# Kernel optimization log

Measured on AMD Instinct MI355X. Metric: run time of the kernel, lower is better.

## Reference

```python
import jax, jax.numpy as jnp
import numpy as np

N0, N1, N2 = 320000, 80000, 16000
E1, E2 = 800000, 160000
IN_C, HID, OUT_C = 128, 64, 48
H1, H2 = 4, 1
NEG_SLOPE = 0.2  # PyG GATv2Conv default leaky_relu slope


def _glorot(key, shape):
    fan_in = shape[0]
    return jax.random.normal(key, shape, jnp.float32) / jnp.sqrt(jnp.asarray(fan_in, jnp.float32))


def setup_inputs() -> dict:
    key = jax.random.key(0)
    ks = jax.random.split(key, 12)
    inp = {
        "x": jax.random.normal(ks[0], (N0, IN_C), jnp.float32),
        # layer 1: GATv2Conv(IN_C -> HID, heads=H1, concat=True)
        "Wl1": _glorot(ks[1], (IN_C, H1 * HID)),
        "bl1": jnp.zeros((H1 * HID,), jnp.float32),
        "Wr1": _glorot(ks[2], (IN_C, H1 * HID)),
        "br1": jnp.zeros((H1 * HID,), jnp.float32),
        "att1": jax.random.normal(ks[3], (H1, HID), jnp.float32) * 0.1,
        "bias1": jnp.zeros((H1 * HID,), jnp.float32),
        # layer 2: GATv2Conv(H1*HID -> OUT_C, heads=H2, concat=False)
        "Wl2": _glorot(ks[4], (H1 * HID, H2 * OUT_C)),
        "bl2": jnp.zeros((H2 * OUT_C,), jnp.float32),
        "Wr2": _glorot(ks[5], (H1 * HID, H2 * OUT_C)),
        "br2": jnp.zeros((H2 * OUT_C,), jnp.float32),
        "att2": jax.random.normal(ks[6], (H2, OUT_C), jnp.float32) * 0.1,
        "bias2": jnp.zeros((OUT_C,), jnp.float32),
        # sampled bipartite edge lists (edge j->i: src index into x_src, dst into x_dst)
        "src1": jax.random.randint(ks[7], (E1,), 0, N0, jnp.int32),
        "dst1": jax.random.randint(ks[8], (E1,), 0, N1, jnp.int32),
        "src2": jax.random.randint(ks[9], (E2,), 0, N1, jnp.int32),
        "dst2": jax.random.randint(ks[10], (E2,), 0, N2, jnp.int32),
        "n1": N1,
        "n2": N2,
    }
    return inp


def gatv2_conv(x_src, x_dst, src, dst, Wl, bl, Wr, br, att, bias, n_dst, concat):
    H, C = att.shape
    xl = (x_src @ Wl + bl).reshape(-1, H, C)   # [N_src, H, C] (source transform)
    xr = (x_dst @ Wr + br).reshape(-1, H, C)   # [N_dst, H, C] (target transform)
    e = xl[src] + xr[dst]                      # [E, H, C]
    e = jnp.where(e > 0, e, NEG_SLOPE * e)     # leaky_relu (GATv2: nonlinearity before att)
    alpha = jnp.einsum('ehc,hc->eh', e, att)   # [E, H] attention logits
    # softmax over edges sharing the same target node
    amax = jax.ops.segment_max(alpha, dst, num_segments=n_dst)
    ex = jnp.exp(alpha - amax[dst])
    denom = jax.ops.segment_sum(ex, dst, num_segments=n_dst)
    w = ex / (denom[dst] + 1e-16)              # [E, H]
    out = jax.ops.segment_sum(xl[src] * w[:, :, None], dst, num_segments=n_dst)  # [N_dst, H, C]
    out = out.reshape(n_dst, H * C) if concat else out.mean(axis=1)
    return out + bias


def reference(x, Wl1, bl1, Wr1, br1, att1, bias1, Wl2, bl2, Wr2, br2, att2, bias2,
              src1, dst1, src2, dst2, n1, n2):
    h = gatv2_conv(x, x[:n1], src1, dst1, Wl1, bl1, Wr1, br1, att1, bias1, n1, True)
    h = jax.nn.relu(h)
    # dropout is identity in eval mode
    h = gatv2_conv(h, h[:n2], src2, dst2, Wl2, bl2, Wr2, br2, att2, bias2, n2, False)
    return jax.nn.log_softmax(h, axis=-1)
```

## Files before the change

kernel.cpp:

```cpp
#include <hip/hip_runtime.h>
#include <hip/hip_bf16.h>

#define N0_  320000
#define N1_  80000
#define N2_  16000
#define INC_ 128
#define HID_ 64
#define H1_  4
#define C1_  256
#define OUT_ 48
#define OUTP_ 64
#define NEG_ 0.2f

typedef __attribute__((ext_vector_type(8))) short bfrag8;
typedef __attribute__((ext_vector_type(4))) float ffrag4;

__device__ __forceinline__ float bf2f(unsigned short u){
  unsigned int v = ((unsigned int)u) << 16;
  return __uint_as_float(v);
}
__device__ __forceinline__ unsigned short f2bf(float f){
  unsigned int u = __float_as_uint(f);
  u += 0x7FFFu + ((u >> 16) & 1u);
  return (unsigned short)(u >> 16);
}
__device__ __forceinline__ void unpack2(unsigned int u, float& lo, float& hi){
  lo = __uint_as_float(u << 16);
  hi = __uint_as_float(u & 0xffff0000u);
}

__global__ void transpose_all(const float* __restrict__ Wl1, const float* __restrict__ Wr1,
                              const float* __restrict__ Wl2, const float* __restrict__ Wr2,
                              unsigned short* __restrict__ Wt1l, unsigned short* __restrict__ Wt1r,
                              unsigned short* __restrict__ Wt2l, unsigned short* __restrict__ Wt2r){
  int idx = blockIdx.x*256 + threadIdx.x;
  if (idx < 32768){ int n = idx >> 7, k = idx & 127; Wt1l[idx] = f2bf(Wl1[k*C1_ + n]); }
  else if (idx < 65536){ int j = idx - 32768; int n = j >> 7, k = j & 127; Wt1r[j] = f2bf(Wr1[k*C1_ + n]); }
  else if (idx < 77824){ int j = idx - 65536; int n = j >> 8, k = j & 255; Wt2l[j] = f2bf(Wl2[k*OUT_ + n]); }
  else if (idx < 90112){ int j = idx - 77824; int n = j >> 8, k = j & 255; Wt2r[j] = f2bf(Wr2[k*OUT_ + n]); }
}

__global__ __launch_bounds__(256, 4) void gemm1_split(
    const float* __restrict__ X,
    const unsigned short* __restrict__ Wtl, const unsigned short* __restrict__ Wtr,
    const float* __restrict__ bl, const float* __restrict__ br,
    unsigned short* __restrict__ outl, unsigned short* __restrict__ outr, int nblk_l)
{
  __shared__ unsigned short Buf[8704];
  const int t = threadIdx.x;
  const int lane = t & 63, wave = t >> 6;
  const bool isR = (int)blockIdx.x >= nblk_l;
  const int row0 = (isR ? (int)blockIdx.x - nblk_l : (int)blockIdx.x) << 6;
  const unsigned short* Wt = isR ? Wtr : Wtl;
  const float* bias = isR ? br : bl;
  unsigned short* out = isR ? outr : outl;
  const int l15 = lane & 15, q = lane >> 4;
  const int wcol = wave << 6;
  const int c4 = t & 31;

  #pragma unroll
  for (int i = 0; i < 8; ++i){
    int r = (i<<3) + (t>>5);
    float4 xv = *(const float4*)(X + ((size_t)(row0 + r) << 7) + (c4<<2));
    ushort4 s; s.x=f2bf(xv.x); s.y=f2bf(xv.y); s.z=f2bf(xv.z); s.w=f2bf(xv.w);
    *(ushort4*)(&Buf[r*136 + (c4<<2)]) = s;
  }
  __syncthreads();

  ffrag4 z = {0.f, 0.f, 0.f, 0.f};
  ffrag4 acc[4][4];
  #pragma unroll
  for (int mt = 0; mt < 4; ++mt)
    #pragma unroll
    for (int nt = 0; nt < 4; ++nt) acc[mt][nt] = z;

  #pragma unroll
  for (int ks = 0; ks < 4; ++ks){
    bfrag8 bfr[4];
    #pragma unroll
    for (int nt = 0; nt < 4; ++nt)
      bfr[nt] = *(const bfrag8*)(Wt + (size_t)(wcol + (nt<<4) + l15)*128 + (ks<<5) + (q<<3));
    #pragma unroll
    for (int mt = 0; mt < 4; ++mt){
      bfrag8 af = *(const bfrag8*)(&Buf[((mt<<4) + l15)*136 + (ks<<5) + (q<<3)]);
      #pragma unroll
      for (int nt = 0; nt < 4; ++nt)
        acc[mt][nt] = __builtin_amdgcn_mfma_f32_16x16x32_bf16(af, bfr[nt], acc[mt][nt], 0, 0, 0);
    }
  }

  float bb[4];
  #pragma unroll
  for (int nt = 0; nt < 4; ++nt) bb[nt] = bias[wcol + (nt<<4) + l15];

  #pragma unroll
  for (int h = 0; h < 2; ++h){
    __syncthreads();
    #pragma unroll
    for (int mh = 0; mh < 2; ++mh){
      int mt = (h<<1) + mh;
      #pragma unroll
      for (int nt = 0; nt < 4; ++nt)
        #pragma unroll
        for (int rg = 0; rg < 4; ++rg)
          Buf[((mh<<4) + (q<<2) + rg)*264 + wcol + (nt<<4) + l15] = f2bf(acc[mt][nt][rg] + bb[nt]);
    }
    __syncthreads();
    #pragma unroll
    for (int i = 0; i < 4; ++i){
      int idx = (i<<8) + t;
      int r = idx >> 5, c = (idx & 31) << 3;
      *(bfrag8*)(out + ((size_t)(row0 + (h<<5) + r) << 8) + c) = *(const bfrag8*)(&Buf[r*264 + c]);
    }
  }
}

__global__ __launch_bounds__(256, 4) void gemm2_split(
    const unsigned short* __restrict__ Hin,
    const unsigned short* __restrict__ Wtl, const unsigned short* __restrict__ Wtr,
    const float* __restrict__ bl, const float* __restrict__ br,
    float* __restrict__ outl, float* __restrict__ outr, int nblk_l)
{
  __shared__ unsigned short As2[64*264];
  const int t = threadIdx.x;
  const int lane = t & 63, wave = t >> 6;
  const bool isR = (int)blockIdx.x >= nblk_l;
  const int row0 = (isR ? (int)blockIdx.x - nblk_l : (int)blockIdx.x) << 6;
  const unsigned short* Wt = isR ? Wtr : Wtl;
  const float* bias = isR ? br : bl;
  float* out = isR ? outr : outl;
  const int l15 = lane & 15, q = lane >> 4;

  #pragma unroll
  for (int i = 0; i < 8; ++i){
    int idx = (i<<8) + t;
    int r = idx >> 5, c = (idx & 31) << 3;
    *(bfrag8*)(&As2[r*264 + c]) = *(const bfrag8*)(Hin + ((size_t)(row0 + r) << 8) + c);
  }
  __syncthreads();

  if (wave < 3){
    bfrag8 bfr[8];
    #pragma unroll
    for (int ks = 0; ks < 8; ++ks)
      bfr[ks] = *(const bfrag8*)(Wt + (size_t)((wave<<4) + l15)*256 + (ks<<5) + (q<<3));
    ffrag4 z = {0.f, 0.f, 0.f, 0.f};
    ffrag4 acc[4] = {z, z, z, z};
    #pragma unroll
    for (int ks = 0; ks < 8; ++ks){
      #pragma unroll
      for (int mt = 0; mt < 4; ++mt){
        bfrag8 af = *(const bfrag8*)(&As2[((mt<<4) + l15)*264 + (ks<<5) + (q<<3)]);
        acc[mt] = __builtin_amdgcn_mfma_f32_16x16x32_bf16(af, bfr[ks], acc[mt], 0, 0, 0);
      }
    }
    int col = (wave<<4) + l15;
    float bb = bias[col];
    #pragma unroll
    for (int mt = 0; mt < 4; ++mt)
      #pragma unroll
      for (int rg = 0; rg < 4; ++rg){
        int row = row0 + (mt<<4) + (q<<2) + rg;
        out[(size_t)row*OUTP_ + col] = acc[mt][rg] + bb;
      }
  } else {
    #pragma unroll
    for (int i = 0; i < 16; ++i){
      int row = row0 + (i<<2) + q;
      out[(size_t)row*OUTP_ + 48 + l15] = 0.f;
    }
  }
}

__global__ void hist_both(const int* __restrict__ dst1, const int* __restrict__ dst2,
                          int* __restrict__ cnt1, int* __restrict__ cnt2, int E1, int E2){
  int i = blockIdx.x*256 + threadIdx.x;
  if (i < E1) atomicAdd(&cnt1[dst1[i]], 1);
  else if (i < E1 + E2) atomicAdd(&cnt2[dst2[i - E1]], 1);
}

__global__ __launch_bounds__(256) void scan_local_both(
    const int* __restrict__ in1, const int* __restrict__ in2,
    int* __restrict__ ex1, int* __restrict__ ex2,
    int* __restrict__ part1, int* __restrict__ part2, int n1, int n2, int nb1){
  __shared__ int s[256];
  const int* in; int* excl; int* partials; int n; int b;
  if ((int)blockIdx.x < nb1){ in = in1; excl = ex1; partials = part1; n = n1; b = blockIdx.x; }
  else { in = in2; excl = ex2; partials = part2; n = n2; b = blockIdx.x - nb1; }
  int t = threadIdx.x, i = b*256 + t;
  int v = (i < n) ? in[i] : 0;
  s[t] = v; __syncthreads();
  #pragma unroll
  for (int off = 1; off < 256; off <<= 1){
    int u = (t >= off) ? s[t-off] : 0;
    __syncthreads();
    s[t] += u; __syncthreads();
  }
  if (i < n) excl[i] = s[t] - v;
  if (t == 255) partials[b] = s[255];
}

__global__ __launch_bounds__(512) void scan_partials_both(
    int* __restrict__ part1, int* __restrict__ part2, int nb1, int nb2){
  __shared__ int s[512];
  int* partials = blockIdx.x ? part2 : part1;
  int nb = blockIdx.x ? nb2 : nb1;
  int t = threadIdx.x;
  int v = (t < nb) ? partials[t] : 0;
  s[t] = v; __syncthreads();
  #pragma unroll
  for (int off = 1; off < 512; off <<= 1){
    int u = (t >= off) ? s[t-off] : 0;
    __syncthreads();
    s[t] += u; __syncthreads();
  }
  if (t < nb) partials[t] = s[t] - v;
}

__global__ void scan_finalize_both(
    int* __restrict__ ex1, int* __restrict__ ex2,
    const int* __restrict__ part1, const int* __restrict__ part2,
    int* __restrict__ cur1, int* __restrict__ cur2, int n1, int n2, int nb1){
  int* excl; const int* partials; int* cursor; int n; int b;
  if ((int)blockIdx.x < nb1){ excl = ex1; partials = part1; cursor = cur1; n = n1; b = blockIdx.x; }
  else { excl = ex2; partials = part2; cursor = cur2; n = n2; b = blockIdx.x - nb1; }
  int i = b*256 + threadIdx.x;
  if (i >= n) return;
  int o = excl[i] + partials[b];
  excl[i] = o; cursor[i] = o;
}

__global__ void scatter_both(const int* __restrict__ src1, const int* __restrict__ dst1,
                             const int* __restrict__ src2, const int* __restrict__ dst2,
                             int* __restrict__ cur1, int* __restrict__ cur2,
                             int* __restrict__ perm1, int* __restrict__ perm2, int E1, int E2){
  int i = blockIdx.x*256 + threadIdx.x;
  if (i < E1){
    int pos = atomicAdd(&cur1[dst1[i]], 1);
    perm1[pos] = src1[i];
  } else if (i < E1 + E2){
    int j = i - E1;
    int pos = atomicAdd(&cur2[dst2[j]], 1);
    perm2[pos] = src2[j];
  }
}

__global__ __launch_bounds__(256) void gat_aggregate1(
    const unsigned short* __restrict__ xl, const unsigned short* __restrict__ xr,
    const int* __restrict__ offsets, const int* __restrict__ counts,
    const int* __restrict__ perm, const float* __restrict__ att,
    const float* __restrict__ bias, unsigned short* __restrict__ hout, int n)
{
  int node = (blockIdx.x << 2) + (threadIdx.x >> 6);
  if (node >= n) return;
  const int lane = threadIdx.x & 63;
  const int slot = lane >> 5;
  const int sub  = lane & 31;
  const int elem = sub << 3;
  const unsigned int ebyte = (unsigned)elem << 1;
  const char* xlb = (const char*)xl;

  const int st = offsets[node], cnt = counts[node];
  uint4 ru = *(const uint4*)(xr + ((size_t)node << 8) + elem);
  float r[8];
  unpack2(ru.x, r[0], r[1]); unpack2(ru.y, r[2], r[3]);
  unpack2(ru.z, r[4], r[5]); unpack2(ru.w, r[6], r[7]);
  float4 al = *(const float4*)(att + elem);
  float4 ah = *(const float4*)(att + elem + 4);
  float a[8] = {al.x, al.y, al.z, al.w, ah.x, ah.y, ah.z, ah.w};

  float acc[8] = {0,0,0,0,0,0,0,0};
  float den = 0.f;

  for (int jb = 0; jb < cnt; jb += 64){
    int m = cnt - jb; if (m > 64) m = 64;
    int pv = (lane < m) ? perm[st + jb + lane] : 0;
    int s_cur = __shfl(pv, slot);
    uint4 xc = *(const uint4*)(xlb + (((unsigned)s_cur << 9) + ebyte));
    for (int j = 0; j < m; j += 2){
      int s_next = __shfl(pv, (j + 2 + slot) & 63);
      uint4 xn = *(const uint4*)(xlb + (((unsigned)s_next << 9) + ebyte));
      float x[8];
      unpack2(xc.x, x[0], x[1]); unpack2(xc.y, x[2], x[3]);
      unpack2(xc.z, x[4], x[5]); unpack2(xc.w, x[6], x[7]);
      float p = 0.f;
      #pragma unroll
      for (int i = 0; i < 8; ++i){
        float v = x[i] + r[i];
        float e = fmaf(NEG_, fminf(v, 0.f), fmaxf(v, 0.f));
        p = fmaf(e, a[i], p);
      }
      p += __shfl_xor(p, 1);
      p += __shfl_xor(p, 2);
      p += __shfl_xor(p, 4);
      float ex = __expf(p);
      ex = (j + slot < m) ? ex : 0.f;
      den += ex;
      #pragma unroll
      for (int i = 0; i < 8; ++i) acc[i] = fmaf(ex, x[i], acc[i]);
      xc = xn;
    }
  }
  den += __shfl_xor(den, 32);
  #pragma unroll
  for (int i = 0; i < 8; ++i) acc[i] += __shfl_xor(acc[i], 32);

  if (slot == 0){
    float w = 1.f / (den + 1e-16f);
    float4 bl = *(const float4*)(bias + elem);
    float4 bh = *(const float4*)(bias + elem + 4);
    float b[8] = {bl.x, bl.y, bl.z, bl.w, bh.x, bh.y, bh.z, bh.w};
    unsigned int o[4];
    #pragma unroll
    for (int i = 0; i < 4; ++i){
      unsigned short lo = f2bf(fmaxf(fmaf(acc[2*i],   w, b[2*i]),   0.f));
      unsigned short hi = f2bf(fmaxf(fmaf(acc[2*i+1], w, b[2*i+1]), 0.f));
      o[i] = (unsigned)lo | ((unsigned)hi << 16);
    }
    *(uint4*)(hout + ((size_t)node << 8) + elem) = make_uint4(o[0], o[1], o[2], o[3]);
  }
}

__global__ __launch_bounds__(256) void gat_aggregate2(
    const float* __restrict__ xl, const float* __restrict__ xr,
    const int* __restrict__ offsets, const int* __restrict__ counts,
    const int* __restrict__ perm, const float* __restrict__ att,
    const float* __restrict__ bias, float* __restrict__ out, int n)
{
  int node = (blockIdx.x << 2) + (threadIdx.x >> 6);
  if (node >= n) return;
  const int lane = threadIdx.x & 63;
  const int slot = lane >> 4;
  const int sub  = lane & 15;
  const bool realc = sub < 12;

  const int st = offsets[node], cnt = counts[node];
  float4 r = *(const float4*)(xr + (size_t)node*OUTP_ + (sub<<2));
  float4 a = realc ? *(const float4*)(att + (sub<<2)) : make_float4(0,0,0,0);
  float4 acc = make_float4(0,0,0,0);
  float den = 0.f;

  for (int jb = 0; jb < cnt; jb += 64){
    int m = cnt - jb; if (m > 64) m = 64;
    int pv = (lane < m) ? perm[st + jb + lane] : 0;
    int s_cur = __shfl(pv, slot);
    float4 xc = *(const float4*)(xl + (size_t)((unsigned)s_cur*OUTP_ + (sub<<2)));
    for (int j = 0; j < m; j += 4){
      int s_next = __shfl(pv, (j + 4 + slot) & 63);
      float4 xn = *(const float4*)(xl + (size_t)((unsigned)s_next*OUTP_ + (sub<<2)));
      float v0 = xc.x + r.x, v1 = xc.y + r.y, v2 = xc.z + r.z, v3 = xc.w + r.w;
      float p;
      p = fmaf(a.x, fmaf(NEG_, fminf(v0,0.f), fmaxf(v0,0.f)), 0.f);
      p = fmaf(a.y, fmaf(NEG_, fminf(v1,0.f), fmaxf(v1,0.f)), p);
      p = fmaf(a.z, fmaf(NEG_, fminf(v2,0.f), fmaxf(v2,0.f)), p);
      p = fmaf(a.w, fmaf(NEG_, fminf(v3,0.f), fmaxf(v3,0.f)), p);
      p += __shfl_xor(p, 1);
      p += __shfl_xor(p, 2);
      p += __shfl_xor(p, 4);
      p += __shfl_xor(p, 8);
      float ex = __expf(p);
      ex = (j + slot < m) ? ex : 0.f;
      den += ex;
      acc.x = fmaf(ex, xc.x, acc.x); acc.y = fmaf(ex, xc.y, acc.y);
      acc.z = fmaf(ex, xc.z, acc.z); acc.w = fmaf(ex, xc.w, acc.w);
      xc = xn;
    }
  }
  den += __shfl_xor(den, 16); den += __shfl_xor(den, 32);
  acc.x += __shfl_xor(acc.x, 16); acc.x += __shfl_xor(acc.x, 32);
  acc.y += __shfl_xor(acc.y, 16); acc.y += __shfl_xor(acc.y, 32);
  acc.z += __shfl_xor(acc.z, 16); acc.z += __shfl_xor(acc.z, 32);
  acc.w += __shfl_xor(acc.w, 16); acc.w += __shfl_xor(acc.w, 32);

  float w = 1.f / (den + 1e-16f);
  float4 b = realc ? *(const float4*)(bias + (sub<<2)) : make_float4(0,0,0,0);
  float v0 = fmaf(acc.x, w, b.x), v1 = fmaf(acc.y, w, b.y);
  float v2 = fmaf(acc.z, w, b.z), v3 = fmaf(acc.w, w, b.w);

  float mx = realc ? fmaxf(fmaxf(v0, v1), fmaxf(v2, v3)) : -3.0e38f;
  mx = fmaxf(mx, __shfl_xor(mx, 1)); mx = fmaxf(mx, __shfl_xor(mx, 2));
  mx = fmaxf(mx, __shfl_xor(mx, 4)); mx = fmaxf(mx, __shfl_xor(mx, 8));
  float es = realc ? (__expf(v0-mx) + __expf(v1-mx) + __expf(v2-mx) + __expf(v3-mx)) : 0.f;
  es += __shfl_xor(es, 1); es += __shfl_xor(es, 2);
  es += __shfl_xor(es, 4); es += __shfl_xor(es, 8);
  float ls = __logf(es);
  if (slot == 0 && realc){
    float4 o = make_float4(v0-mx-ls, v1-mx-ls, v2-mx-ls, v3-mx-ls);
    *(float4*)(out + (size_t)node*OUT_ + (sub<<2)) = o;
  }
}

extern "C" void kernel_launch(void* const* d_in, const int* in_sizes, int n_in,
                              void* d_out, int out_size, void* d_ws, size_t ws_size,
                              hipStream_t stream)
{
  const float* x    = (const float*)d_in[0];
  const float* Wl1  = (const float*)d_in[1];
  const float* bl1  = (const float*)d_in[2];
  const float* Wr1  = (const float*)d_in[3];
  const float* br1  = (const float*)d_in[4];
  const float* att1 = (const float*)d_in[5];
  const float* bias1= (const float*)d_in[6];
  const float* Wl2  = (const float*)d_in[7];
  const float* bl2  = (const float*)d_in[8];
  const float* Wr2  = (const float*)d_in[9];
  const float* br2  = (const float*)d_in[10];
  const float* att2 = (const float*)d_in[11];
  const float* bias2= (const float*)d_in[12];
  const int* src1 = (const int*)d_in[13];
  const int* dst1 = (const int*)d_in[14];
  const int* src2 = (const int*)d_in[15];
  const int* dst2 = (const int*)d_in[16];
  const int E1 = in_sizes[13];
  const int E2 = in_sizes[15];
  (void)n_in; (void)out_size; (void)ws_size;

  char* ws = (char*)d_ws;
  unsigned short* xl1  = (unsigned short*)(ws + 0LL);
  unsigned short* xr1  = (unsigned short*)(ws + 163840000LL);
  unsigned short* hbuf = (unsigned short*)(ws + 204800000LL);
  float* xl2p   = (float*)(ws + 245760000LL);
  float* xr2p   = (float*)(ws + 266240000LL);
  int*   perm1  = (int*)  (ws + 270336000LL);
  int*   perm2  = (int*)  (ws + 273536000LL);
  int*   cnt1   = (int*)  (ws + 274176000LL);
  int*   cnt2   = (int*)  (ws + 274496000LL);
  int*   off1   = (int*)  (ws + 274560000LL);
  int*   cur1   = (int*)  (ws + 274880000LL);
  int*   off2   = (int*)  (ws + 275200000LL);
  int*   cur2   = (int*)  (ws + 275264000LL);
  int*   part1  = (int*)  (ws + 275328000LL);
  int*   part2  = (int*)  (ws + 275330048LL);
  unsigned short* Wt1l = (unsigned short*)(ws + 275332096LL);
  unsigned short* Wt1r = (unsigned short*)(ws + 275397632LL);
  unsigned short* Wt2l = (unsigned short*)(ws + 275463168LL);
  unsigned short* Wt2r = (unsigned short*)(ws + 275487744LL);

  hipMemsetAsync(ws + 274176000LL, 0, 384000LL, stream);

  const int nb1 = (N1_ + 255) / 256;
  const int nb2 = (N2_ + 255) / 256;

  transpose_all<<<352, 256, 0, stream>>>(Wl1, Wr1, Wl2, Wr2, Wt1l, Wt1r, Wt2l, Wt2r);

  hist_both         <<<(E1+E2+255)/256, 256, 0, stream>>>(dst1, dst2, cnt1, cnt2, E1, E2);
  scan_local_both   <<<nb1+nb2, 256, 0, stream>>>(cnt1, cnt2, off1, off2, part1, part2, N1_, N2_, nb1);
  scan_partials_both<<<2, 512, 0, stream>>>(part1, part2, nb1, nb2);
  scan_finalize_both<<<nb1+nb2, 256, 0, stream>>>(off1, off2, part1, part2, cur1, cur2, N1_, N2_, nb1);
  scatter_both      <<<(E1+E2+255)/256, 256, 0, stream>>>(src1, dst1, src2, dst2,
                                                          cur1, cur2, perm1, perm2, E1, E2);

  gemm1_split<<<N0_/64 + N1_/64, 256, 0, stream>>>(x, Wt1l, Wt1r, bl1, br1, xl1, xr1, N0_/64);

  gat_aggregate1<<<(N1_+3)/4, 256, 0, stream>>>(xl1, xr1, off1, cnt1, perm1,
                                                att1, bias1, hbuf, N1_);

  gemm2_split<<<N1_/64 + N2_/64, 256, 0, stream>>>(hbuf, Wt2l, Wt2r, bl2, br2, xl2p, xr2p, N1_/64);

  gat_aggregate2<<<(N2_+3)/4, 256, 0, stream>>>(xl2p, xr2p, off2, cnt2, perm2,
                                                att2, bias2, (float*)d_out, N2_);
}
```

Before: 545.6 us.

## Restructure GEMMs: persistent multi-tile blocks with register-resident weights, direct A loads

The layer-1 GEMM now uses 512-thread blocks that each process five 64-row tiles. Each wave keeps its 32-column weight fragments in registers across tiles and loads X straight from global memory into MFMA fragments, so the shared-memory staging pass is gone. The layer-2 GEMM also drops its shared-memory A staging and reads bf16 rows directly from global memory. The aim is to cut LDS traffic, syncs and repeated weight loads. The cost is uncoalesced, strided global loads for the A operand, and every wave re-reads the same rows.

```diff
diff --git a/kernel.cpp b/kernel.cpp
--- a/kernel.cpp
+++ b/kernel.cpp
@@ -40,88 +40,83 @@
   else if (idx < 90112){ int j = idx - 77824; int n = j >> 8, k = j & 255; Wt2r[j] = f2bf(Wr2[k*OUT_ + n]); }
 }
 
-__global__ __launch_bounds__(256, 4) void gemm1_split(
+__global__ __launch_bounds__(512, 4) void gemm1_v3(
     const float* __restrict__ X,
     const unsigned short* __restrict__ Wtl, const unsigned short* __restrict__ Wtr,
     const float* __restrict__ bl, const float* __restrict__ br,
-    unsigned short* __restrict__ outl, unsigned short* __restrict__ outr, int nblk_l)
+    unsigned short* __restrict__ outl, unsigned short* __restrict__ outr,
+    int nblk_l, int tiles_per_blk)
 {
-  __shared__ unsigned short Buf[8704];
+  __shared__ unsigned short Cs[64][264];
   const int t = threadIdx.x;
   const int lane = t & 63, wave = t >> 6;
   const bool isR = (int)blockIdx.x >= nblk_l;
-  const int row0 = (isR ? (int)blockIdx.x - nblk_l : (int)blockIdx.x) << 6;
+  const int blk = isR ? (int)blockIdx.x - nblk_l : (int)blockIdx.x;
   const unsigned short* Wt = isR ? Wtr : Wtl;
   const float* bias = isR ? br : bl;
   unsigned short* out = isR ? outr : outl;
   const int l15 = lane & 15, q = lane >> 4;
-  const int wcol = wave << 6;
-  const int c4 = t & 31;
-
+  const int wcol = wave << 5;
+
+  bfrag8 bfr[2][4];
   #pragma unroll
-  for (int i = 0; i < 8; ++i){
-    int r = (i<<3) + (t>>5);
-    float4 xv = *(const float4*)(X + ((size_t)(row0 + r) << 7) + (c4<<2));
-    ushort4 s; s.x=f2bf(xv.x); s.y=f2bf(xv.y); s.z=f2bf(xv.z); s.w=f2bf(xv.w);
-    *(ushort4*)(&Buf[r*136 + (c4<<2)]) = s;
-  }
-  __syncthreads();
-
-  ffrag4 z = {0.f, 0.f, 0.f, 0.f};
-  ffrag4 acc[4][4];
-  #pragma unroll
-  for (int mt = 0; mt < 4; ++mt)
-    #pragma unroll
-    for (int nt = 0; nt < 4; ++nt) acc[mt][nt] = z;
-
-  #pragma unroll
-  for (int ks = 0; ks < 4; ++ks){
-    bfrag8 bfr[4];
-    #pragma unroll
-    for (int nt = 0; nt < 4; ++nt)
-      bfr[nt] = *(const bfrag8*)(Wt + (size_t)(wcol + (nt<<4) + l15)*128 + (ks<<5) + (q<<3));
-    #pragma unroll
-    for (int mt = 0; mt < 4; ++mt){
-      bfrag8 af = *(const bfrag8*)(&Buf[((mt<<4) + l15)*136 + (ks<<5) + (q<<3)]);
-      #pragma unroll
-      for (int nt = 0; nt < 4; ++nt)
-        acc[mt][nt] = __builtin_amdgcn_mfma_f32_16x16x32_bf16(af, bfr[nt], acc[mt][nt], 0, 0, 0);
-    }
-  }
-
-  float bb[4];
-  #pragma unroll
-  for (int nt = 0; nt < 4; ++nt) bb[nt] = bias[wcol + (nt<<4) + l15];
-
-  #pragma unroll
-  for (int h = 0; h < 2; ++h){
+  for (int nt = 0; nt < 2; ++nt)
+    #pragma unroll
+    for (int ks = 0; ks < 4; ++ks)
+      bfr[nt][ks] = *(const bfrag8*)(Wt + (size_t)(wcol + (nt<<4) + l15)*128 + (ks<<5) + (q<<3));
+  float bb[2] = { bias[wcol + l15], bias[wcol + 16 + l15] };
+
+  for (int tile = 0; tile < tiles_per_blk; ++tile){
+    const int row0 = (blk*tiles_per_blk + tile) << 6;
+    ffrag4 z = {0.f,0.f,0.f,0.f};
+    ffrag4 acc[4][2];
+    #pragma unroll
+    for (int mt = 0; mt < 4; ++mt){ acc[mt][0] = z; acc[mt][1] = z; }
+
+    #pragma unroll
+    for (int ks = 0; ks < 4; ++ks){
+      bfrag8 af[4];
+      #pragma unroll
+      for (int mt = 0; mt < 4; ++mt){
+        const float* ap = X + ((size_t)(row0 + (mt<<4) + l15) << 7) + (ks<<5) + (q<<3);
+        float4 a0 = *(const float4*)(ap);
+        float4 a1 = *(const float4*)(ap + 4);
+        bfrag8 f;
+        f[0]=(short)f2bf(a0.x); f[1]=(short)f2bf(a0.y); f[2]=(short)f2bf(a0.z); f[3]=(short)f2bf(a0.w);
+        f[4]=(short)f2bf(a1.x); f[5]=(short)f2bf(a1.y); f[6]=(short)f2bf(a1.z); f[7]=(short)f2bf(a1.w);
+        af[mt] = f;
+      }
+      #pragma unroll
+      for (int mt = 0; mt < 4; ++mt){
+        acc[mt][0] = __builtin_amdgcn_mfma_f32_16x16x32_bf16(af[mt], bfr[0][ks], acc[mt][0], 0, 0, 0);
+        acc[mt][1] = __builtin_amdgcn_mfma_f32_16x16x32_bf16(af[mt], bfr[1][ks], acc[mt][1], 0, 0, 0);
+      }
+    }
+
     __syncthreads();
     #pragma unroll
-    for (int mh = 0; mh < 2; ++mh){
-      int mt = (h<<1) + mh;
-      #pragma unroll
-      for (int nt = 0; nt < 4; ++nt)
+    for (int mt = 0; mt < 4; ++mt)
+      #pragma unroll
+      for (int nt = 0; nt < 2; ++nt)
         #pragma unroll
         for (int rg = 0; rg < 4; ++rg)
-          Buf[((mh<<4) + (q<<2) + rg)*264 + wcol + (nt<<4) + l15] = f2bf(acc[mt][nt][rg] + bb[nt]);
-    }
+          Cs[(mt<<4) + (q<<2) + rg][wcol + (nt<<4) + l15] = f2bf(acc[mt][nt][rg] + bb[nt]);
     __syncthreads();
     #pragma unroll
     for (int i = 0; i < 4; ++i){
-      int idx = (i<<8) + t;
+      int idx = (i<<9) + t;
       int r = idx >> 5, c = (idx & 31) << 3;
-      *(bfrag8*)(out + ((size_t)(row0 + (h<<5) + r) << 8) + c) = *(const bfrag8*)(&Buf[r*264 + c]);
-    }
-  }
-}
-
-__global__ __launch_bounds__(256, 4) void gemm2_split(
+      *(bfrag8*)(out + ((size_t)(row0 + r) << 8) + c) = *(const bfrag8*)(&Cs[r][c]);
+    }
+  }
+}
+
+__global__ __launch_bounds__(256) void gemm2_v2(
     const unsigned short* __restrict__ Hin,
     const unsigned short* __restrict__ Wtl, const unsigned short* __restrict__ Wtr,
     const float* __restrict__ bl, const float* __restrict__ br,
     float* __restrict__ outl, float* __restrict__ outr, int nblk_l)
 {
-  __shared__ unsigned short As2[64*264];
   const int t = threadIdx.x;
   const int lane = t & 63, wave = t >> 6;
   const bool isR = (int)blockIdx.x >= nblk_l;
@@ -131,37 +126,29 @@
   float* out = isR ? outr : outl;
   const int l15 = lane & 15, q = lane >> 4;
 
-  #pragma unroll
-  for (int i = 0; i < 8; ++i){
-    int idx = (i<<8) + t;
-    int r = idx >> 5, c = (idx & 31) << 3;
-    *(bfrag8*)(&As2[r*264 + c]) = *(const bfrag8*)(Hin + ((size_t)(row0 + r) << 8) + c);
-  }
-  __syncthreads();
-
   if (wave < 3){
     bfrag8 bfr[8];
     #pragma unroll
     for (int ks = 0; ks < 8; ++ks)
       bfr[ks] = *(const bfrag8*)(Wt + (size_t)((wave<<4) + l15)*256 + (ks<<5) + (q<<3));
-    ffrag4 z = {0.f, 0.f, 0.f, 0.f};
+    ffrag4 z = {0.f,0.f,0.f,0.f};
     ffrag4 acc[4] = {z, z, z, z};
     #pragma unroll
     for (int ks = 0; ks < 8; ++ks){
       #pragma unroll
       for (int mt = 0; mt < 4; ++mt){
-        bfrag8 af = *(const bfrag8*)(&As2[((mt<<4) + l15)*264 + (ks<<5) + (q<<3)]);
+        bfrag8 af = *(const bfrag8*)(Hin + ((size_t)(row0 + (mt<<4) + l15) << 8) + (ks<<5) + (q<<3));
         acc[mt] = __builtin_amdgcn_mfma_f32_16x16x32_bf16(af, bfr[ks], acc[mt], 0, 0, 0);
       }
     }
     int col = (wave<<4) + l15;
-    float bb = bias[col];
+    float bbv = bias[col];
     #pragma unroll
     for (int mt = 0; mt < 4; ++mt)
       #pragma unroll
       for (int rg = 0; rg < 4; ++rg){
         int row = row0 + (mt<<4) + (q<<2) + rg;
-        out[(size_t)row*OUTP_ + col] = acc[mt][rg] + bb;
+        out[(size_t)row*OUTP_ + col] = acc[mt][rg] + bbv;
       }
   } else {
     #pragma unroll
@@ -450,12 +437,12 @@
   scatter_both      <<<(E1+E2+255)/256, 256, 0, stream>>>(src1, dst1, src2, dst2,
                                                           cur1, cur2, perm1, perm2, E1, E2);
 
-  gemm1_split<<<N0_/64 + N1_/64, 256, 0, stream>>>(x, Wt1l, Wt1r, bl1, br1, xl1, xr1, N0_/64);
+  gemm1_v3<<<1250, 512, 0, stream>>>(x, Wt1l, Wt1r, bl1, br1, xl1, xr1, 1000, 5);
 
   gat_aggregate1<<<(N1_+3)/4, 256, 0, stream>>>(xl1, xr1, off1, cnt1, perm1,
                                                 att1, bias1, hbuf, N1_);
 
-  gemm2_split<<<N1_/64 + N2_/64, 256, 0, stream>>>(hbuf, Wt2l, Wt2r, bl2, br2, xl2p, xr2p, N1_/64);
+  gemm2_v2<<<N1_/64 + N2_/64, 256, 0, stream>>>(hbuf, Wt2l, Wt2r, bl2, br2, xl2p, xr2p, N1_/64);
 
   gat_aggregate2<<<(N2_+3)/4, 256, 0, stream>>>(xl2p, xr2p, off2, cnt2, perm2,
                                                 att2, bias2, (float*)d_out, N2_);
```

Measured after the change: 644.3 us. +18.1%, slower.

## Make layer-1 GEMM persistent over row tiles with prefetch; drop LDS staging in GEMM2

Applied to the files above, without the earlier changes.

The first-layer projection GEMM now has each block process five consecutive 64-row tiles. Each block keeps its weight fragments in registers, prefetches the next X tile into registers during the MFMA phase, and uses a separate LDS buffer for output staging. The second GEMM reads A fragments straight from global memory instead of staging them through shared memory. This trades more registers and lower occupancy for fewer weight reloads and overlap of loads with compute. Direct global fragment loads in GEMM2 may be less coalesced.

```diff
diff --git a/kernel.cpp b/kernel.cpp
--- a/kernel.cpp
+++ b/kernel.cpp
@@ -40,88 +40,116 @@
   else if (idx < 90112){ int j = idx - 77824; int n = j >> 8, k = j & 255; Wt2r[j] = f2bf(Wr2[k*OUT_ + n]); }
 }
 
-__global__ __launch_bounds__(256, 4) void gemm1_split(
+__global__ __launch_bounds__(256, 2) void gemm1_v4(
     const float* __restrict__ X,
     const unsigned short* __restrict__ Wtl, const unsigned short* __restrict__ Wtr,
     const float* __restrict__ bl, const float* __restrict__ br,
-    unsigned short* __restrict__ outl, unsigned short* __restrict__ outr, int nblk_l)
+    unsigned short* __restrict__ outl, unsigned short* __restrict__ outr,
+    int nblk_l, int tiles)
 {
-  __shared__ unsigned short Buf[8704];
+  __shared__ unsigned short As[64*136];
+  __shared__ unsigned short Csh[32*264];
   const int t = threadIdx.x;
   const int lane = t & 63, wave = t >> 6;
   const bool isR = (int)blockIdx.x >= nblk_l;
-  const int row0 = (isR ? (int)blockIdx.x - nblk_l : (int)blockIdx.x) << 6;
+  const int blk = isR ? (int)blockIdx.x - nblk_l : (int)blockIdx.x;
   const unsigned short* Wt = isR ? Wtr : Wtl;
   const float* bias = isR ? br : bl;
   unsigned short* out = isR ? outr : outl;
   const int l15 = lane & 15, q = lane >> 4;
   const int wcol = wave << 6;
-  const int c4 = t & 31;
+  const int r8 = t >> 5;
+  const int c32 = t & 31;
+
+  int row0 = (blk * tiles) << 6;
+  float4 pf[8];
+  #pragma unroll
+  for (int i = 0; i < 8; ++i)
+    pf[i] = *(const float4*)(X + ((size_t)(row0 + (i<<3) + r8) << 7) + (c32<<2));
+
+  bfrag8 bfr[4][4];
+  #pragma unroll
+  for (int nt = 0; nt < 4; ++nt)
+    #pragma unroll
+    for (int ks = 0; ks < 4; ++ks)
+      bfr[nt][ks] = *(const bfrag8*)(Wt + (size_t)(wcol + (nt<<4) + l15)*128 + (ks<<5) + (q<<3));
+  float bb[4];
+  #pragma unroll
+  for (int nt = 0; nt < 4; ++nt) bb[nt] = bias[wcol + (nt<<4) + l15];
 
   #pragma unroll
   for (int i = 0; i < 8; ++i){
-    int r = (i<<3) + (t>>5);
-    float4 xv = *(const float4*)(X + ((size_t)(row0 + r) << 7) + (c4<<2));
-    ushort4 s; s.x=f2bf(xv.x); s.y=f2bf(xv.y); s.z=f2bf(xv.z); s.w=f2bf(xv.w);
-    *(ushort4*)(&Buf[r*136 + (c4<<2)]) = s;
+    ushort4 s; s.x=f2bf(pf[i].x); s.y=f2bf(pf[i].y); s.z=f2bf(pf[i].z); s.w=f2bf(pf[i].w);
+    *(ushort4*)(&As[((i<<3) + r8)*136 + (c32<<2)]) = s;
   }
   __syncthreads();
 
-  ffrag4 z = {0.f, 0.f, 0.f, 0.f};
-  ffrag4 acc[4][4];
-  #pragma unroll
-  for (int mt = 0; mt < 4; ++mt)
-    #pragma unroll
-    for (int nt = 0; nt < 4; ++nt) acc[mt][nt] = z;
-
-  #pragma unroll
-  for (int ks = 0; ks < 4; ++ks){
-    bfrag8 bfr[4];
-    #pragma unroll
-    for (int nt = 0; nt < 4; ++nt)
-      bfr[nt] = *(const bfrag8*)(Wt + (size_t)(wcol + (nt<<4) + l15)*128 + (ks<<5) + (q<<3));
-    #pragma unroll
-    for (int mt = 0; mt < 4; ++mt){
-      bfrag8 af = *(const bfrag8*)(&Buf[((mt<<4) + l15)*136 + (ks<<5) + (q<<3)]);
-      #pragma unroll
-      for (int nt = 0; nt < 4; ++nt)
-        acc[mt][nt] = __builtin_amdgcn_mfma_f32_16x16x32_bf16(af, bfr[nt], acc[mt][nt], 0, 0, 0);
-    }
-  }
-
-  float bb[4];
-  #pragma unroll
-  for (int nt = 0; nt < 4; ++nt) bb[nt] = bias[wcol + (nt<<4) + l15];
-
-  #pragma unroll
-  for (int h = 0; h < 2; ++h){
+  for (int tile = 0; tile < tiles; ++tile){
+    row0 = (blk * tiles + tile) << 6;
+    const bool havenext = (tile + 1 < tiles);
+    if (havenext){
+      int rown = row0 + 64;
+      #pragma unroll
+      for (int i = 0; i < 8; ++i)
+        pf[i] = *(const float4*)(X + ((size_t)(rown + (i<<3) + r8) << 7) + (c32<<2));
+    }
+
+    ffrag4 z = {0.f,0.f,0.f,0.f};
+    ffrag4 acc[4][4];
+    #pragma unroll
+    for (int mt = 0; mt < 4; ++mt)
+      #pragma unroll
+      for (int nt = 0; nt < 4; ++nt) acc[mt][nt] = z;
+
+    #pragma unroll
+    for (int mt = 0; mt < 4; ++mt)
+      #pragma unroll
+      for (int ks = 0; ks < 4; ++ks){
+        bfrag8 af = *(const bfrag8*)(&As[((mt<<4) + l15)*136 + (ks<<5) + (q<<3)]);
+        #pragma unroll
+        for (int nt = 0; nt < 4; ++nt)
+          acc[mt][nt] = __builtin_amdgcn_mfma_f32_16x16x32_bf16(af, bfr[nt][ks], acc[mt][nt], 0, 0, 0);
+      }
+
     __syncthreads();
-    #pragma unroll
-    for (int mh = 0; mh < 2; ++mh){
-      int mt = (h<<1) + mh;
-      #pragma unroll
-      for (int nt = 0; nt < 4; ++nt)
+    if (havenext){
+      #pragma unroll
+      for (int i = 0; i < 8; ++i){
+        ushort4 s; s.x=f2bf(pf[i].x); s.y=f2bf(pf[i].y); s.z=f2bf(pf[i].z); s.w=f2bf(pf[i].w);
+        *(ushort4*)(&As[((i<<3) + r8)*136 + (c32<<2)]) = s;
+      }
+    }
+
+    #pragma unroll
+    for (int h = 0; h < 2; ++h){
+      if (h) __syncthreads();
+      #pragma unroll
+      for (int mh = 0; mh < 2; ++mh){
+        int mt = (h<<1) + mh;
         #pragma unroll
-        for (int rg = 0; rg < 4; ++rg)
-          Buf[((mh<<4) + (q<<2) + rg)*264 + wcol + (nt<<4) + l15] = f2bf(acc[mt][nt][rg] + bb[nt]);
+        for (int nt = 0; nt < 4; ++nt)
+          #pragma unroll
+          for (int rg = 0; rg < 4; ++rg)
+            Csh[((mh<<4) + (q<<2) + rg)*264 + wcol + (nt<<4) + l15] = f2bf(acc[mt][nt][rg] + bb[nt]);
+      }
+      __syncthreads();
+      #pragma unroll
+      for (int i = 0; i < 4; ++i){
+        int idx = (i<<8) + t;
+        int r = idx >> 5, c = (idx & 31) << 3;
+        *(bfrag8*)(out + ((size_t)(row0 + (h<<5) + r) << 8) + c) = *(const bfrag8*)(&Csh[r*264 + c]);
+      }
     }
     __syncthreads();
-    #pragma unroll
-    for (int i = 0; i < 4; ++i){
-      int idx = (i<<8) + t;
-      int r = idx >> 5, c = (idx & 31) << 3;
-      *(bfrag8*)(out + ((size_t)(row0 + (h<<5) + r) << 8) + c) = *(const bfrag8*)(&Buf[r*264 + c]);
-    }
-  }
-}
-
-__global__ __launch_bounds__(256, 4) void gemm2_split(
+  }
+}
+
+__global__ __launch_bounds__(256) void gemm2_v2(
     const unsigned short* __restrict__ Hin,
     const unsigned short* __restrict__ Wtl, const unsigned short* __restrict__ Wtr,
     const float* __restrict__ bl, const float* __restrict__ br,
     float* __restrict__ outl, float* __restrict__ outr, int nblk_l)
 {
-  __shared__ unsigned short As2[64*264];
   const int t = threadIdx.x;
   const int lane = t & 63, wave = t >> 6;
   const bool isR = (int)blockIdx.x >= nblk_l;
@@ -131,37 +159,29 @@
   float* out = isR ? outr : outl;
   const int l15 = lane & 15, q = lane >> 4;
 
-  #pragma unroll
-  for (int i = 0; i < 8; ++i){
-    int idx = (i<<8) + t;
-    int r = idx >> 5, c = (idx & 31) << 3;
-    *(bfrag8*)(&As2[r*264 + c]) = *(const bfrag8*)(Hin + ((size_t)(row0 + r) << 8) + c);
-  }
-  __syncthreads();
-
   if (wave < 3){
     bfrag8 bfr[8];
     #pragma unroll
     for (int ks = 0; ks < 8; ++ks)
       bfr[ks] = *(const bfrag8*)(Wt + (size_t)((wave<<4) + l15)*256 + (ks<<5) + (q<<3));
-    ffrag4 z = {0.f, 0.f, 0.f, 0.f};
+    ffrag4 z = {0.f,0.f,0.f,0.f};
     ffrag4 acc[4] = {z, z, z, z};
     #pragma unroll
     for (int ks = 0; ks < 8; ++ks){
       #pragma unroll
       for (int mt = 0; mt < 4; ++mt){
-        bfrag8 af = *(const bfrag8*)(&As2[((mt<<4) + l15)*264 + (ks<<5) + (q<<3)]);
+        bfrag8 af = *(const bfrag8*)(Hin + ((size_t)(row0 + (mt<<4) + l15) << 8) + (ks<<5) + (q<<3));
         acc[mt] = __builtin_amdgcn_mfma_f32_16x16x32_bf16(af, bfr[ks], acc[mt], 0, 0, 0);
       }
     }
     int col = (wave<<4) + l15;
-    float bb = bias[col];
+    float bbv = bias[col];
     #pragma unroll
     for (int mt = 0; mt < 4; ++mt)
       #pragma unroll
       for (int rg = 0; rg < 4; ++rg){
         int row = row0 + (mt<<4) + (q<<2) + rg;
-        out[(size_t)row*OUTP_ + col] = acc[mt][rg] + bb;
+        out[(size_t)row*OUTP_ + col] = acc[mt][rg] + bbv;
       }
   } else {
     #pragma unroll
@@ -450,12 +470,12 @@
   scatter_both      <<<(E1+E2+255)/256, 256, 0, stream>>>(src1, dst1, src2, dst2,
                                                           cur1, cur2, perm1, perm2, E1, E2);
 
-  gemm1_split<<<N0_/64 + N1_/64, 256, 0, stream>>>(x, Wt1l, Wt1r, bl1, br1, xl1, xr1, N0_/64);
+  gemm1_v4<<<1250, 256, 0, stream>>>(x, Wt1l, Wt1r, bl1, br1, xl1, xr1, 1000, 5);
 
   gat_aggregate1<<<(N1_+3)/4, 256, 0, stream>>>(xl1, xr1, off1, cnt1, perm1,
                                                 att1, bias1, hbuf, N1_);
 
-  gemm2_split<<<N1_/64 + N2_/64, 256, 0, stream>>>(hbuf, Wt2l, Wt2r, bl2, br2, xl2p, xr2p, N1_/64);
+  gemm2_v2<<<N1_/64 + N2_/64, 256, 0, stream>>>(hbuf, Wt2l, Wt2r, bl2, br2, xl2p, xr2p, N1_/64);
 
   gat_aggregate2<<<(N2_+3)/4, 256, 0, stream>>>(xl2p, xr2p, off2, cnt2, perm2,
                                                 att2, bias2, (float*)d_out, N2_);
```

Measured after the change: 553.5 us. About the same (+1.5%).
